# Kernel tuning notes

Measured on AMD Instinct MI355X. Metric: run time of the kernel, lower is better.

Reference implementation:

```python
import jax, jax.numpy as jnp
import numpy as np

D_MODEL, KAN_HIDDEN, NUM, K = 1024, 128, 3, 3  # grid_size=3, spline order k=3
GRID_RANGE = (-1.0, 1.0)


def make_grid(in_dim):
    # extended grid: num+1 interior knots padded by k steps of h on each side -> num+1+2k points
    h = (GRID_RANGE[1] - GRID_RANGE[0]) / NUM
    g = jnp.arange(-K, NUM + K + 1, dtype=jnp.float32) * h + GRID_RANGE[0]  # [num+1+2k]
    return jnp.broadcast_to(g, (in_dim, g.shape[0]))  # [in_dim, G]


def b_splines(x, grid):
    # Cox-de-Boor recursion. x: [N, D], grid: [D, G] -> basis [N, D, G-1-K]
    xg = x[:, :, None]  # [N, D, 1]
    B = ((xg >= grid[None, :, :-1]) & (xg < grid[None, :, 1:])).astype(x.dtype)
    for d in range(1, K + 1):
        left = (xg - grid[None, :, : -(d + 1)]) / (grid[:, d:-1] - grid[:, : -(d + 1)])[None]
        right = (grid[None, :, d + 1:] - xg) / (grid[:, d + 1:] - grid[:, 1:-d])[None]
        B = left * B[:, :, :-1] + right * B[:, :, 1:]
    return B  # [N, D, NUM+K]


def kan_layer(x, grid, coef, scale_base, scale_sp):
    # y[n,i,o] = scale_base[i,o]*silu(x[n,i]) + scale_sp[i,o]*sum_g B[n,i,g]*coef[i,o,g]; out = y.sum(i)
    B = b_splines(x, grid)  # [N, in, NUM+K]
    spline = jnp.einsum('nig,iog->no', B, coef * scale_sp[:, :, None])
    base = jnp.einsum('ni,io->no', jax.nn.silu(x), scale_base)
    return base + spline  # [N, out]


def setup_inputs() -> dict:
    key = jax.random.key(0)
    ks = jax.random.split(key, 7)
    s = 0.1  # small init scale for spline coefficients, matching noisy init spirit
    return {
        'x': jax.random.normal(ks[0], (4, 4096, D_MODEL), dtype=jnp.float32),
        'coef1': jax.random.normal(ks[1], (D_MODEL, KAN_HIDDEN, NUM + K), dtype=jnp.float32) * s,
        'scale_base1': jax.random.normal(ks[2], (D_MODEL, KAN_HIDDEN), dtype=jnp.float32),
        'scale_sp1': jnp.ones((D_MODEL, KAN_HIDDEN), dtype=jnp.float32),
        'coef2': jax.random.normal(ks[3], (KAN_HIDDEN, D_MODEL, NUM + K), dtype=jnp.float32) * s,
        'scale_base2': jax.random.normal(ks[4], (KAN_HIDDEN, D_MODEL), dtype=jnp.float32),
        'scale_sp2': jnp.ones((KAN_HIDDEN, D_MODEL), dtype=jnp.float32),
    }


def reference(x, coef1, scale_base1, scale_sp1, coef2, scale_base2, scale_sp2):
    b, s, d = x.shape
    xf = x.reshape(-1, d)  # [N, d_model]
    g1 = make_grid(D_MODEL)
    g2 = make_grid(KAN_HIDDEN)
    y1 = kan_layer(xf, g1, coef1, scale_base1, scale_sp1)   # [N, kan_hidden]
    y2 = kan_layer(y1, g2, coef2, scale_base2, scale_sp2)   # [N, d_model]
    return y2.reshape(b, s, d)
```

## Files before the change

### kernel.cpp

```cpp
#include <hip/hip_runtime.h>
#include <stdint.h>

typedef float f32x4 __attribute__((ext_vector_type(4)));
typedef __bf16 bf16x8 __attribute__((ext_vector_type(8)));
typedef __bf16 bf16x2 __attribute__((ext_vector_type(2)));
typedef unsigned short ushort4v __attribute__((ext_vector_type(4)));

#define NROW 16384
#define DM   1024
#define HID  128
#define K1   8192
#define K2   1024
#define KSPLIT 4

__device__ __forceinline__ unsigned short f2bf(float f) {
  unsigned u = __builtin_bit_cast(unsigned, f);
  u += 0x7fffu + ((u >> 16) & 1u);
  return (unsigned short)(u >> 16);
}

__device__ __forceinline__ uint32_t pk2(float lo, float hi) {
  bf16x2 v;
  v[0] = (__bf16)lo;
  v[1] = (__bf16)hi;
  return __builtin_bit_cast(uint32_t, v);
}

__device__ __forceinline__ void g2l16(const void* g, void* l) {
  __builtin_amdgcn_global_load_lds(
      (const __attribute__((address_space(1))) unsigned int*)g,
      (__attribute__((address_space(3))) unsigned int*)l, 16, 0, 0);
}

__device__ __forceinline__ bf16x8 expand8(float v) {
  const float t = (v + 3.0f) * 1.5f;
  const float cf = floorf(t);
  const float u = t - cf;
  int c = (int)cf;
  c = c < -1 ? -1 : c;
  c = c > 9 ? 9 : c;
  const float u2 = u * u, u3 = u2 * u, omu = 1.0f - u;
  const float p0 = u3 * (1.0f / 6.0f);
  float p1 = __builtin_fmaf(0.5f, u, 1.0f / 6.0f);
  p1 = __builtin_fmaf(0.5f, u2, p1);
  p1 = __builtin_fmaf(-0.5f, u3, p1);
  float p2 = __builtin_fmaf(0.5f, u3, 4.0f / 6.0f);
  p2 = p2 - u2;
  const float p3 = (omu * omu) * (omu * (1.0f / 6.0f));
  const uint64_t W = (uint64_t)pk2(p3, p2) | ((uint64_t)pk2(p1, p0) << 32);
  const int sa = (c - 2) * 16;
  const int sl = sa & 63;
  const uint64_t t1 = W << sl;
  const uint64_t t2 = (W >> (63 - sl)) >> 1;
  const uint64_t t3 = W >> ((-sa) & 63);
  const uint64_t L = sa < 0 ? t3 : (sa < 64 ? t1 : 0);
  const uint64_t H = sa < 0 ? 0  : (sa < 64 ? t2 : t1);
  const float e = __expf(-v);
  const float s = v * __builtin_amdgcn_rcpf(1.0f + e);
  const uint32_t su = __builtin_bit_cast(uint32_t, s);
  const uint32_t shf_bits = su & 0xffff0000u;
  const float slo_f = s - __builtin_bit_cast(float, shf_bits);
  const uint32_t slo = (uint32_t)__builtin_bit_cast(unsigned short, (__bf16)slo_f);
  const uint32_t w0 = ((uint32_t)L & 0xffff0000u) | (shf_bits >> 16);
  const uint32_t w1 = (uint32_t)(L >> 32);
  const uint32_t w2 = (uint32_t)H;
  const uint32_t w3 = ((uint32_t)(H >> 32) & 0xffffu) | (slo << 16);
  union { uint4 q; bf16x8 b; } r;
  r.q = (uint4){w0, w1, w2, w3};
  return r.b;
}

__global__ void kan_prep_w1(const float* __restrict__ c1, const float* __restrict__ sb1,
                            const float* __restrict__ sp1, unsigned short* __restrict__ w1p) {
  const int t = blockIdx.x * 256 + threadIdx.x;
  const int o = t >> 10, i = t & 1023;
  const float sb = sb1[i * HID + o], sp = sp1[i * HID + o];
  const float* cf = c1 + (size_t)(i * HID + o) * 6;
  union { uint4 u; unsigned short h[8]; } r;
  const unsigned short b = f2bf(sb);
  r.h[0] = b; r.h[7] = b;
#pragma unroll
  for (int g = 0; g < 6; ++g) r.h[g + 1] = f2bf(cf[g] * sp);
  const int kh = i >> 8, iq = i & 255;
  const int wk = iq >> 7, gg = (iq >> 5) & 3, it = iq & 31;
  const int lane = gg * 16 + (o & 15), ni = o >> 4;
  const size_t flat = (size_t)kh * 262144 + it * 8192 + wk * 4096 + ni * 512 + lane * 8;
  *(uint4*)(w1p + flat) = r.u;
}

__global__ void kan_prep_w2(const float* __restrict__ c2, const float* __restrict__ sb2,
                            const float* __restrict__ sp2, unsigned short* __restrict__ w2t) {
  const int t = blockIdx.x * 256 + threadIdx.x;
  const int o = t >> 7, i = t & 127;
  const float sb = sb2[i * DM + o], sp = sp2[i * DM + o];
  const float* cf = c2 + (size_t)(i * DM + o) * 6;
  union { uint4 u; unsigned short h[8]; } r;
  const unsigned short b = f2bf(sb);
  r.h[0] = b; r.h[7] = b;
#pragma unroll
  for (int g = 0; g < 6; ++g) r.h[g + 1] = f2bf(cf[g] * sp);
  *(uint4*)(w2t + (size_t)o * K2 + i * 8) = r.u;
}

__global__ __launch_bounds__(256, 2) void kan_gemm1(
    const float* __restrict__ x, const unsigned short* __restrict__ w1p,
    unsigned short* __restrict__ yq) {
  __shared__ __align__(16) char lds[65536];
  const int tid = threadIdx.x;
  const int lane = tid & 63, w = tid >> 6;
  const int wm = w >> 1, wk = w & 1;
  const int mt = blockIdx.x >> 2, kh = blockIdx.x & 3;
  const int m0 = mt * 128;
  const int g = lane >> 4;

  f32x4 acc[4][8];
#pragma unroll
  for (int a = 0; a < 4; ++a)
#pragma unroll
    for (int b = 0; b < 8; ++b) acc[a][b] = (f32x4){0.f, 0.f, 0.f, 0.f};

  const int arow = m0 + wm * 64 + (lane & 15);
  const float* xp[4];
#pragma unroll
  for (int mi = 0; mi < 4; ++mi)
    xp[mi] = x + (size_t)(arow + mi * 16) * DM + kh * 256 + wk * 128 + g * 32;

  const unsigned short* bp = w1p + (size_t)kh * 262144 + wk * 4096 + lane * 8;

  f32x4 xq[4], xn[4];
#pragma unroll
  for (int mi = 0; mi < 4; ++mi) xq[mi] = *(const f32x4*)(xp[mi]);

  for (int c4 = 0; c4 < 8; ++c4) {
    if (c4 + 1 < 8) {
#pragma unroll
      for (int mi = 0; mi < 4; ++mi) xn[mi] = *(const f32x4*)(xp[mi] + (c4 + 1) * 4);
    }
#pragma unroll
    for (int it4 = 0; it4 < 4; ++it4) {
      const int it = c4 * 4 + it4;
      bf16x8 b[8], af[4];
#pragma unroll
      for (int ni = 0; ni < 8; ++ni)
        b[ni] = *(const bf16x8*)(bp + (size_t)it * 8192 + ni * 512);
#pragma unroll
      for (int mi = 0; mi < 4; ++mi) af[mi] = expand8(xq[mi][it4]);
#pragma unroll
      for (int mi = 0; mi < 4; ++mi)
#pragma unroll
        for (int ni = 0; ni < 8; ++ni)
          acc[mi][ni] = __builtin_amdgcn_mfma_f32_16x16x32_bf16(af[mi], b[ni], acc[mi][ni], 0, 0, 0);
    }
#pragma unroll
    for (int mi = 0; mi < 4; ++mi) xq[mi] = xn[mi];
  }

  if (wk == 1) {
    char* r = lds + wm * 32768;
#pragma unroll
    for (int mi = 0; mi < 4; ++mi)
#pragma unroll
      for (int ni = 0; ni < 8; ++ni)
        *(f32x4*)(r + (mi * 8 + ni) * 1024 + lane * 16) = acc[mi][ni];
  }
  __syncthreads();
  if (wk == 0) {
    const char* r = lds + wm * 32768;
    unsigned short* yb = yq + (size_t)kh * NROW * HID;
#pragma unroll
    for (int mi = 0; mi < 4; ++mi)
#pragma unroll
      for (int ni = 0; ni < 8; ++ni) {
        f32x4 o = *(const f32x4*)(r + (mi * 8 + ni) * 1024 + lane * 16);
        o += acc[mi][ni];
        const int col = ni * 16 + (lane & 15);
#pragma unroll
        for (int rr = 0; rr < 4; ++rr) {
          const int row = wm * 64 + mi * 16 + (lane >> 4) * 4 + rr;
          yb[(size_t)(m0 + row) * HID + col] = __builtin_bit_cast(unsigned short, (__bf16)o[rr]);
        }
      }
  }
}

__global__ void kan_combine(const unsigned short* __restrict__ yq, unsigned short* __restrict__ a2) {
  const size_t i4 = ((size_t)blockIdx.x * 256 + threadIdx.x) * 4;
  float v[4] = {0.f, 0.f, 0.f, 0.f};
#pragma unroll
  for (int h = 0; h < KSPLIT; ++h) {
    ushort4v q = *(const ushort4v*)(yq + (size_t)h * NROW * HID + i4);
#pragma unroll
    for (int j = 0; j < 4; ++j)
      v[j] += __builtin_bit_cast(float, (uint32_t)q[j] << 16);
  }
#pragma unroll
  for (int j = 0; j < 4; ++j)
    *(bf16x8*)(a2 + (i4 + j) * 8) = expand8(v[j]);
}

__global__ __launch_bounds__(256, 2) void kan_gemm2(
    const unsigned short* __restrict__ a2, const unsigned short* __restrict__ w2t,
    float* __restrict__ out) {
  __shared__ __align__(16) unsigned short lds[2 * 16384];
  const int tid = threadIdx.x;
  const int lane = tid & 63, w = tid >> 6;
  const int wm = w >> 1, wn = w & 1;
  const int mt = blockIdx.x & 127, nt = blockIdx.x >> 7;
  const int m0 = mt * 128, n0 = nt * 128;

  f32x4 acc[4][4];
#pragma unroll
  for (int a = 0; a < 4; ++a)
#pragma unroll
    for (int b = 0; b < 4; ++b) acc[a][b] = (f32x4){0.f, 0.f, 0.f, 0.f};

  auto stage = [&](int kt, int buf) {
#pragma unroll
    for (int q = 0; q < 4; ++q) {
      const int r = (w * 4 + q) * 8 + (lane >> 3);
      const int slot = (lane & 7) ^ (lane >> 3);
      g2l16(a2 + (size_t)(m0 + r) * K2 + kt * 64 + slot * 8,
            (char*)lds + buf * 32768 + (w * 4 + q) * 1024);
      g2l16(w2t + (size_t)(n0 + r) * K2 + kt * 64 + slot * 8,
            (char*)lds + buf * 32768 + 16384 + (w * 4 + q) * 1024);
    }
  };

  stage(0, 0);
  for (int kt = 0; kt < 16; ++kt) {
    const int cur = kt & 1;
    if (kt + 1 < 16) {
      stage(kt + 1, cur ^ 1);
      asm volatile("s_waitcnt vmcnt(8)" ::: "memory");
    } else {
      asm volatile("s_waitcnt vmcnt(0)" ::: "memory");
    }
    __builtin_amdgcn_sched_barrier(0);
    __builtin_amdgcn_s_barrier();
    const char* ab = (const char*)lds + cur * 32768;
    const char* bb = ab + 16384;
#pragma unroll
    for (int ks = 0; ks < 2; ++ks) {
      bf16x8 af[4], bfr[4];
#pragma unroll
      for (int mi = 0; mi < 4; ++mi) {
        const int row = wm * 64 + mi * 16 + (lane & 15);
        af[mi] = *(const bf16x8*)(ab + ((row * 128 + ks * 64 + (lane >> 4) * 16) ^ ((row & 7) << 4)));
      }
#pragma unroll
      for (int ni = 0; ni < 4; ++ni) {
        const int col = wn * 64 + ni * 16 + (lane & 15);
        bfr[ni] = *(const bf16x8*)(bb + ((col * 128 + ks * 64 + (lane >> 4) * 16) ^ ((col & 7) << 4)));
      }
#pragma unroll
      for (int mi = 0; mi < 4; ++mi)
#pragma unroll
        for (int ni = 0; ni < 4; ++ni)
          acc[mi][ni] = __builtin_amdgcn_mfma_f32_16x16x32_bf16(af[mi], bfr[ni], acc[mi][ni], 0, 0, 0);
    }
    __builtin_amdgcn_s_barrier();
  }

#pragma unroll
  for (int mi = 0; mi < 4; ++mi)
#pragma unroll
    for (int r = 0; r < 4; ++r) {
      const int row = wm * 64 + mi * 16 + (lane >> 4) * 4 + r;
#pragma unroll
      for (int ni = 0; ni < 4; ++ni) {
        const int col = wn * 64 + ni * 16 + (lane & 15);
        out[(size_t)(m0 + row) * DM + n0 + col] = acc[mi][ni][r];
      }
    }
}

extern "C" void kernel_launch(void* const* d_in, const int* in_sizes, int n_in,
                              void* d_out, int out_size, void* d_ws, size_t ws_size,
                              hipStream_t stream) {
  const float* x   = (const float*)d_in[0];
  const float* c1  = (const float*)d_in[1];
  const float* sb1 = (const float*)d_in[2];
  const float* sp1 = (const float*)d_in[3];
  const float* c2  = (const float*)d_in[4];
  const float* sb2 = (const float*)d_in[5];
  const float* sp2 = (const float*)d_in[6];
  float* out = (float*)d_out;

  unsigned short* w1p = (unsigned short*)d_ws;
  unsigned short* w2t = w1p + (size_t)HID * K1;
  unsigned short* a2  = w2t + (size_t)DM * K2;
  unsigned short* yq  = a2 + (size_t)NROW * K2;

  kan_prep_w1<<<512, 256, 0, stream>>>(c1, sb1, sp1, w1p);
  kan_prep_w2<<<512, 256, 0, stream>>>(c2, sb2, sp2, w2t);
  kan_gemm1<<<512, 256, 0, stream>>>(x, w1p, yq);
  kan_combine<<<NROW * HID / 1024, 256, 0, stream>>>(yq, a2);
  kan_gemm2<<<(NROW / 128) * (DM / 128), 256, 0, stream>>>(a2, w2t, out);
}
```

Measured before the change: 151.8 us.

## Split gemm1 N dimension across 8 waves to cut accumulator registers

Moves the first GEMM kernel from 4 to 8 waves per block. Each wave now covers half of the 128 output columns, so its accumulator tile shrinks from 4x8 to 4x4 fragments. The x loads become float2 per step and the K loop is restructured to match. Block indices are also remapped so paired blocks sharing a k-half sit next to each other, and the LDS k-split reduction now runs in two rounds to fit in 32KB. The goal is higher occupancy with lower register pressure. The cost is that each x element is loaded and expanded twice per block, plus extra barriers.

```diff
diff --git a/kernel.cpp b/kernel.cpp
--- a/kernel.cpp
+++ b/kernel.cpp
@@ -102,22 +102,24 @@
   *(uint4*)(w2t + (size_t)o * K2 + i * 8) = r.u;
 }
 
-__global__ __launch_bounds__(256, 2) void kan_gemm1(
+__global__ __launch_bounds__(512, 4) void kan_gemm1(
     const float* __restrict__ x, const unsigned short* __restrict__ w1p,
     unsigned short* __restrict__ yq) {
-  __shared__ __align__(16) char lds[65536];
+  __shared__ __align__(16) char lds[32768];
   const int tid = threadIdx.x;
   const int lane = tid & 63, w = tid >> 6;
-  const int wm = w >> 1, wk = w & 1;
-  const int mt = blockIdx.x >> 2, kh = blockIdx.x & 3;
+  const int wm = w >> 2, wn = (w >> 1) & 1, wk = w & 1;
+  const int bid = blockIdx.x;
+  const int kh = (bid & 7) >> 1;
+  const int mt = ((bid >> 3) << 1) | (bid & 1);
   const int m0 = mt * 128;
   const int g = lane >> 4;
 
-  f32x4 acc[4][8];
+  f32x4 acc[4][4];
 #pragma unroll
   for (int a = 0; a < 4; ++a)
 #pragma unroll
-    for (int b = 0; b < 8; ++b) acc[a][b] = (f32x4){0.f, 0.f, 0.f, 0.f};
+    for (int b = 0; b < 4; ++b) acc[a][b] = (f32x4){0.f, 0.f, 0.f, 0.f};
 
   const int arow = m0 + wm * 64 + (lane & 15);
   const float* xp[4];
@@ -125,61 +127,67 @@
   for (int mi = 0; mi < 4; ++mi)
     xp[mi] = x + (size_t)(arow + mi * 16) * DM + kh * 256 + wk * 128 + g * 32;
 
-  const unsigned short* bp = w1p + (size_t)kh * 262144 + wk * 4096 + lane * 8;
-
-  f32x4 xq[4], xn[4];
-#pragma unroll
-  for (int mi = 0; mi < 4; ++mi) xq[mi] = *(const f32x4*)(xp[mi]);
-
-  for (int c4 = 0; c4 < 8; ++c4) {
-    if (c4 + 1 < 8) {
-#pragma unroll
-      for (int mi = 0; mi < 4; ++mi) xn[mi] = *(const f32x4*)(xp[mi] + (c4 + 1) * 4);
-    }
-#pragma unroll
-    for (int it4 = 0; it4 < 4; ++it4) {
-      const int it = c4 * 4 + it4;
-      bf16x8 b[8], af[4];
-#pragma unroll
-      for (int ni = 0; ni < 8; ++ni)
+  const unsigned short* bp =
+      w1p + (size_t)kh * 262144 + wk * 4096 + wn * 2048 + lane * 8;
+
+  float2 xq[4], xn[4];
+#pragma unroll
+  for (int mi = 0; mi < 4; ++mi) xq[mi] = *(const float2*)(xp[mi]);
+
+  for (int c2 = 0; c2 < 16; ++c2) {
+    if (c2 + 1 < 16) {
+#pragma unroll
+      for (int mi = 0; mi < 4; ++mi) xn[mi] = *(const float2*)(xp[mi] + (c2 + 1) * 2);
+    }
+#pragma unroll
+    for (int it2 = 0; it2 < 2; ++it2) {
+      const int it = c2 * 2 + it2;
+      bf16x8 b[4], af[4];
+#pragma unroll
+      for (int ni = 0; ni < 4; ++ni)
         b[ni] = *(const bf16x8*)(bp + (size_t)it * 8192 + ni * 512);
 #pragma unroll
-      for (int mi = 0; mi < 4; ++mi) af[mi] = expand8(xq[mi][it4]);
-#pragma unroll
-      for (int mi = 0; mi < 4; ++mi)
-#pragma unroll
-        for (int ni = 0; ni < 8; ++ni)
+      for (int mi = 0; mi < 4; ++mi)
+        af[mi] = expand8(it2 ? xq[mi].y : xq[mi].x);
+#pragma unroll
+      for (int mi = 0; mi < 4; ++mi)
+#pragma unroll
+        for (int ni = 0; ni < 4; ++ni)
           acc[mi][ni] = __builtin_amdgcn_mfma_f32_16x16x32_bf16(af[mi], b[ni], acc[mi][ni], 0, 0, 0);
     }
 #pragma unroll
     for (int mi = 0; mi < 4; ++mi) xq[mi] = xn[mi];
   }
 
-  if (wk == 1) {
-    char* r = lds + wm * 32768;
-#pragma unroll
-    for (int mi = 0; mi < 4; ++mi)
-#pragma unroll
-      for (int ni = 0; ni < 8; ++ni)
-        *(f32x4*)(r + (mi * 8 + ni) * 1024 + lane * 16) = acc[mi][ni];
-  }
-  __syncthreads();
-  if (wk == 0) {
-    const char* r = lds + wm * 32768;
-    unsigned short* yb = yq + (size_t)kh * NROW * HID;
-#pragma unroll
-    for (int mi = 0; mi < 4; ++mi)
-#pragma unroll
-      for (int ni = 0; ni < 8; ++ni) {
-        f32x4 o = *(const f32x4*)(r + (mi * 8 + ni) * 1024 + lane * 16);
-        o += acc[mi][ni];
-        const int col = ni * 16 + (lane & 15);
-#pragma unroll
-        for (int rr = 0; rr < 4; ++rr) {
-          const int row = wm * 64 + mi * 16 + (lane >> 4) * 4 + rr;
-          yb[(size_t)(m0 + row) * HID + col] = __builtin_bit_cast(unsigned short, (__bf16)o[rr]);
+  unsigned short* yb = yq + (size_t)kh * NROW * HID;
+#pragma unroll
+  for (int rnd = 0; rnd < 2; ++rnd) {
+    if ((w >> 2) == rnd && (w & 1) == 1) {
+      char* r = lds + ((w >> 1) & 1) * 16384;
+#pragma unroll
+      for (int mi = 0; mi < 4; ++mi)
+#pragma unroll
+        for (int ni = 0; ni < 4; ++ni)
+          *(f32x4*)(r + (mi * 4 + ni) * 1024 + lane * 16) = acc[mi][ni];
+    }
+    __syncthreads();
+    if ((w >> 2) == rnd && (w & 1) == 0) {
+      const char* r = lds + ((w >> 1) & 1) * 16384;
+#pragma unroll
+      for (int mi = 0; mi < 4; ++mi)
+#pragma unroll
+        for (int ni = 0; ni < 4; ++ni) {
+          f32x4 o = *(const f32x4*)(r + (mi * 4 + ni) * 1024 + lane * 16);
+          o += acc[mi][ni];
+          const int col = wn * 64 + ni * 16 + (lane & 15);
+#pragma unroll
+          for (int rr = 0; rr < 4; ++rr) {
+            const int row = wm * 64 + mi * 16 + (lane >> 4) * 4 + rr;
+            yb[(size_t)(m0 + row) * HID + col] = __builtin_bit_cast(unsigned short, (__bf16)o[rr]);
+          }
         }
-      }
+    }
+    __syncthreads();
   }
 }
 
@@ -293,7 +301,7 @@
 
   kan_prep_w1<<<512, 256, 0, stream>>>(c1, sb1, sp1, w1p);
   kan_prep_w2<<<512, 256, 0, stream>>>(c2, sb2, sp2, w2t);
-  kan_gemm1<<<512, 256, 0, stream>>>(x, w1p, yq);
+  kan_gemm1<<<512, 512, 0, stream>>>(x, w1p, yq);
   kan_combine<<<NROW * HID / 1024, 256, 0, stream>>>(yq, a2);
   kan_gemm2<<<(NROW / 128) * (DM / 128), 256, 0, stream>>>(a2, w2t, out);
 }
```

New measurement: 342.3 us. +125.4%, slower.
